# Kernel optimization log

Hardware: AMD Instinct MI355X
Metric: run time of the kernel (lower is better)

The kernel has to match this reference:

```python
import jax, jax.numpy as jnp
import numpy as np

N_FINE = 200000   # data.num_nodes (fine level)
N_COARSE = 50000  # nodes kept at coarse level
C = 128           # feature channels


def setup_inputs() -> dict:
    key = jax.random.key(0)
    x = jax.random.normal(key, (N_COARSE, 2, C, 2), dtype=jnp.float32)
    rng = np.random.default_rng(0)
    # coarse nodes are a subset of fine node ids
    unpool_nodes = np.sort(rng.permutation(N_FINE)[:N_COARSE]).astype(np.int32)
    # each fine node has exactly one unpool edge from some coarse node
    edge_src = unpool_nodes[rng.integers(0, N_COARSE, N_FINE)].astype(np.int32)
    edge_dst = rng.permutation(N_FINE).astype(np.int32)
    unpool_edges = jnp.asarray(np.stack([edge_src, edge_dst], axis=0))
    # unit complex parallel-transport rotations per edge
    theta = rng.uniform(0.0, 2.0 * np.pi, N_FINE).astype(np.float32)
    unpool_connection = jnp.asarray(np.stack([np.cos(theta), np.sin(theta)], axis=1))
    return {
        "x": x,
        "unpool_connection": unpool_connection,
        "unpool_nodes": jnp.asarray(unpool_nodes),
        "unpool_edges": unpool_edges,
        "num_nodes": N_FINE,
    }


def reference(x, unpool_connection, unpool_nodes, unpool_edges, num_nodes):
    n_coarse = unpool_nodes.shape[0]
    # unpool_map[fine_id_of_coarse_node] = coarse row index
    unpool_map = jnp.zeros((num_nodes,), dtype=jnp.int32).at[unpool_nodes].set(
        jnp.arange(n_coarse, dtype=jnp.int32))
    # gather coarse features per edge, scatter to fine node slots
    gathered = x[unpool_map[unpool_edges[0]]]               # [E, 2, C, 2]
    new_x = jnp.zeros((num_nodes,) + x.shape[1:], x.dtype).at[unpool_edges[1]].set(gathered)
    # align connection with fine node order (edges[1] is a permutation)
    connection = unpool_connection[jnp.argsort(unpool_edges[1])]  # [N, 2]
    # complex product on the order-1 stream: (a_re + i a_im) * (b_re - i b_im)
    a_re = new_x[:, 1, :, 0]            # [N, C]
    a_im = new_x[:, 1, :, 1]
    b_re = connection[:, None, 0]       # [N, 1]
    b_im = -connection[:, None, 1]
    out_re = a_re * b_re - a_im * b_im
    out_im = a_re * b_im + a_im * b_re
    new_x = new_x.at[:, 1, :, 0].set(out_re).at[:, 1, :, 1].set(out_im)
    return new_x
```

## Files before the change

kernel.cpp:

```cpp
#include <hip/hip_runtime.h>


__global__ __launch_bounds__(256) void PTU_build_map_kernel(
    const int* __restrict__ nodes,
    int*       __restrict__ map,
    int n_coarse)
{
    int i = blockIdx.x * 256 + threadIdx.x;
    if (i < n_coarse) map[nodes[i]] = i;
}

__global__ __launch_bounds__(256) void ParallelTransportUnpool_87582973100651_kernel(
    const float4* __restrict__ x,
    const float2* __restrict__ conn,
    const int*    __restrict__ map,
    const int*    __restrict__ edge_src,
    const int*    __restrict__ edge_dst,
    float4*       __restrict__ out,
    int n_fine)
{
    int wv = __builtin_amdgcn_readfirstlane(threadIdx.x >> 6);
    int e  = blockIdx.x * 4 + wv;
    if (e >= n_fine) return;
    int lane = threadIdx.x & 63;

    int s = __builtin_amdgcn_readfirstlane(edge_src[e]);
    int d = __builtin_amdgcn_readfirstlane(edge_dst[e]);
    int c = __builtin_amdgcn_readfirstlane(map[s]);

    const float4* __restrict__ xr = x + (size_t)c * 128;
    float4 v0 = xr[lane];
    float4 v1 = xr[lane + 64];
    float2 b  = conn[e];

    float br = b.x, bi = -b.y;
    float4 r;
    r.x = v1.x * br - v1.y * bi;
    r.y = v1.x * bi + v1.y * br;
    r.z = v1.z * br - v1.w * bi;
    r.w = v1.z * bi + v1.w * br;

    float4* __restrict__ orow = out + (size_t)d * 128;
    orow[lane]      = v0;
    orow[lane + 64] = r;
}

__global__ __launch_bounds__(256) void PTU_bsearch_kernel(
    const float4* __restrict__ x,
    const float2* __restrict__ conn,
    const int*    __restrict__ nodes,
    const int*    __restrict__ edge_src,
    const int*    __restrict__ edge_dst,
    float4*       __restrict__ out,
    int n_fine, int n_coarse)
{
    int e = blockIdx.x * 2 + (threadIdx.x >> 7);
    if (e >= n_fine) return;
    int lane = threadIdx.x & 127;

    int s = edge_src[e];
    int d = edge_dst[e];

    int lo = 0, hi = n_coarse - 1;
    while (lo < hi) {
        int mid = (lo + hi) >> 1;
        if (nodes[mid] < s) lo = mid + 1; else hi = mid;
    }
    int c = lo;

    float4 v = x[(size_t)c * 128 + lane];
    if (lane >= 64) {
        float2 b = conn[e];
        float br = b.x, bi = -b.y;
        float4 r;
        r.x = v.x * br - v.y * bi;
        r.y = v.x * bi + v.y * br;
        r.z = v.z * br - v.w * bi;
        r.w = v.z * bi + v.w * br;
        v = r;
    }
    out[(size_t)d * 128 + lane] = v;
}

extern "C" void kernel_launch(void* const* d_in, const int* in_sizes, int n_in,
                              void* d_out, int out_size, void* d_ws, size_t ws_size,
                              hipStream_t stream) {
    const float4* x     = (const float4*)d_in[0];
    const float2* conn  = (const float2*)d_in[1];
    const int*    nodes = (const int*)d_in[2];
    const int*    edges = (const int*)d_in[3];

    const int n_coarse = in_sizes[2];
    const int n_fine   = in_sizes[3] / 2;

    const int* edge_src = edges;
    const int* edge_dst = edges + n_fine;

    float4* out = (float4*)d_out;

    if (ws_size >= (size_t)n_fine * sizeof(int)) {
        int* map = (int*)d_ws;
        int mblocks = (n_coarse + 255) / 256;
        PTU_build_map_kernel<<<mblocks, 256, 0, stream>>>(nodes, map, n_coarse);

        int blocks = (n_fine + 3) / 4;
        ParallelTransportUnpool_87582973100651_kernel<<<blocks, 256, 0, stream>>>(
            x, conn, map, edge_src, edge_dst, out, n_fine);
    } else {
        int blocks = (n_fine + 1) / 2;
        PTU_bsearch_kernel<<<blocks, 256, 0, stream>>>(
            x, conn, nodes, edge_src, edge_dst, out, n_fine, n_coarse);
    }
}
```

Baseline: 519.8 us.

## Invert scatter to gather via per-row info table and use nontemporal stores

Adds a pre-pass that builds a per-destination-row record (coarse index plus connection) indexed by edge_dst. The main kernel then walks output rows in order, so its writes are sequential instead of scattered by a permutation. The output stores are also marked nontemporal to avoid polluting the cache. The cost is an extra small kernel launch and a workspace table of size n_fine float4, which needs a larger workspace to take this path.

```diff
diff --git a/kernel.cpp b/kernel.cpp
--- a/kernel.cpp
+++ b/kernel.cpp
@@ -1,5 +1,7 @@
 #include <hip/hip_runtime.h>
 
+
+typedef float v4f __attribute__((ext_vector_type(4)));
 
 __global__ __launch_bounds__(256) void PTU_build_map_kernel(
     const int* __restrict__ nodes,
@@ -10,7 +12,57 @@
     if (i < n_coarse) map[nodes[i]] = i;
 }
 
+__global__ __launch_bounds__(256) void PTU_build_rowinfo_kernel(
+    const int*    __restrict__ map,
+    const float2* __restrict__ conn,
+    const int*    __restrict__ edge_src,
+    const int*    __restrict__ edge_dst,
+    float4*       __restrict__ rowinfo,
+    int n_fine)
+{
+    int e = blockIdx.x * 256 + threadIdx.x;
+    if (e >= n_fine) return;
+    int s = edge_src[e];
+    int d = edge_dst[e];
+    int c = map[s];
+    float2 b = conn[e];
+    rowinfo[d] = make_float4(__int_as_float(c), b.x, b.y, 0.0f);
+}
+
 __global__ __launch_bounds__(256) void ParallelTransportUnpool_87582973100651_kernel(
+    const float4* __restrict__ x,
+    const float4* __restrict__ rowinfo,
+    float4*       __restrict__ out,
+    int n_fine)
+{
+    int wv = threadIdx.x >> 6;
+    int r  = blockIdx.x * 4 + wv;
+    if (r >= n_fine) return;
+    int lane = threadIdx.x & 63;
+
+    float4 info = rowinfo[r];
+    int   c  = __builtin_amdgcn_readfirstlane(__float_as_int(info.x));
+    float br = info.y;
+    float bi = -info.z;
+
+    const float4* __restrict__ xr = x + (size_t)c * 128;
+    float4 v0 = xr[lane];
+    float4 v1 = xr[lane + 64];
+
+    float4 t;
+    t.x = v1.x * br - v1.y * bi;
+    t.y = v1.x * bi + v1.y * br;
+    t.z = v1.z * br - v1.w * bi;
+    t.w = v1.z * bi + v1.w * br;
+
+    float4* orow = out + (size_t)r * 128;
+    v4f nv0 = { v0.x, v0.y, v0.z, v0.w };
+    v4f nv1 = { t.x,  t.y,  t.z,  t.w  };
+    __builtin_nontemporal_store(nv0, reinterpret_cast<v4f*>(&orow[lane]));
+    __builtin_nontemporal_store(nv1, reinterpret_cast<v4f*>(&orow[lane + 64]));
+}
+
+__global__ __launch_bounds__(256) void PTU_map_scatter_kernel(
     const float4* __restrict__ x,
     const float2* __restrict__ conn,
     const int*    __restrict__ map,
@@ -34,15 +86,15 @@
     float2 b  = conn[e];
 
     float br = b.x, bi = -b.y;
-    float4 r;
-    r.x = v1.x * br - v1.y * bi;
-    r.y = v1.x * bi + v1.y * br;
-    r.z = v1.z * br - v1.w * bi;
-    r.w = v1.z * bi + v1.w * br;
+    float4 t;
+    t.x = v1.x * br - v1.y * bi;
+    t.y = v1.x * bi + v1.y * br;
+    t.z = v1.z * br - v1.w * bi;
+    t.w = v1.z * bi + v1.w * br;
 
-    float4* __restrict__ orow = out + (size_t)d * 128;
+    float4* orow = out + (size_t)d * 128;
     orow[lane]      = v0;
-    orow[lane + 64] = r;
+    orow[lane + 64] = t;
 }
 
 __global__ __launch_bounds__(256) void PTU_bsearch_kernel(
@@ -72,12 +124,12 @@
     if (lane >= 64) {
         float2 b = conn[e];
         float br = b.x, bi = -b.y;
-        float4 r;
-        r.x = v.x * br - v.y * bi;
-        r.y = v.x * bi + v.y * br;
-        r.z = v.z * br - v.w * bi;
-        r.w = v.z * bi + v.w * br;
-        v = r;
+        float4 t;
+        t.x = v.x * br - v.y * bi;
+        t.y = v.x * bi + v.y * br;
+        t.z = v.z * br - v.w * bi;
+        t.w = v.z * bi + v.w * br;
+        v = t;
     }
     out[(size_t)d * 128 + lane] = v;
 }
@@ -98,13 +150,30 @@
 
     float4* out = (float4*)d_out;
 
-    if (ws_size >= (size_t)n_fine * sizeof(int)) {
+    const size_t need_full = (size_t)n_fine * sizeof(float4) + (size_t)n_fine * sizeof(int);
+    const size_t need_map  = (size_t)n_fine * sizeof(int);
+
+    if (ws_size >= need_full) {
+        float4* rowinfo = (float4*)d_ws;
+        int*    map     = (int*)(rowinfo + n_fine);
+
+        int mblocks = (n_coarse + 255) / 256;
+        PTU_build_map_kernel<<<mblocks, 256, 0, stream>>>(nodes, map, n_coarse);
+
+        int eblocks = (n_fine + 255) / 256;
+        PTU_build_rowinfo_kernel<<<eblocks, 256, 0, stream>>>(
+            map, conn, edge_src, edge_dst, rowinfo, n_fine);
+
+        int blocks = (n_fine + 3) / 4;
+        ParallelTransportUnpool_87582973100651_kernel<<<blocks, 256, 0, stream>>>(
+            x, rowinfo, out, n_fine);
+    } else if (ws_size >= need_map) {
         int* map = (int*)d_ws;
         int mblocks = (n_coarse + 255) / 256;
         PTU_build_map_kernel<<<mblocks, 256, 0, stream>>>(nodes, map, n_coarse);
 
         int blocks = (n_fine + 3) / 4;
-        ParallelTransportUnpool_87582973100651_kernel<<<blocks, 256, 0, stream>>>(
+        PTU_map_scatter_kernel<<<blocks, 256, 0, stream>>>(
             x, conn, map, edge_src, edge_dst, out, n_fine);
     } else {
         int blocks = (n_fine + 1) / 2;
```

Measured after the change: 503.7 us. 1.03x faster.
